# Performance work log

Measured on AMD Instinct MI355X. Metric: run time of the kernel, lower is better.

The kernel has to match this reference:

```python
import jax, jax.numpy as jnp
import numpy as np

N = 50000
E = 800000
IN, HID, OUT = 256, 128, 64
BN_EPS = 1e-5

def sage(x, src, dst, Wl, bl, Wr):
    # PyG SAGEConv (aggr='mean'): lin_l(mean_j x_j) + lin_r(x_root)
    agg = jax.ops.segment_sum(x[src], dst, num_segments=N)
    deg = jax.ops.segment_sum(jnp.ones((src.shape[0], 1), x.dtype), dst, num_segments=N)
    mean_agg = agg / jnp.maximum(deg, 1.0)
    return mean_agg @ Wl + bl + x @ Wr

def bn_eval(x, gamma, beta):
    # eval-mode BatchNorm1d with running_mean=0, running_var=1
    return x * (gamma / jnp.sqrt(1.0 + BN_EPS)) + beta

def setup_inputs() -> dict:
    key = jax.random.key(0)
    ks = jax.random.split(key, 16)
    g = lambda k, shp, s: jax.random.normal(k, shp, jnp.float32) * s
    inp = {
        'x': g(ks[0], (N, IN), 1.0),
        'edge_index': jax.random.randint(ks[1], (2, E), 0, N, jnp.int32),
        'eps': g(ks[2], (10, N, OUT), 1.0),
        'W1l': g(ks[3], (IN, HID), 0.06), 'b1': jnp.zeros((HID,), jnp.float32), 'W1r': g(ks[4], (IN, HID), 0.06),
        'g1': jnp.ones((HID,), jnp.float32), 'be1': jnp.zeros((HID,), jnp.float32),
        'W2l': g(ks[5], (HID, 2 * HID), 0.09), 'b2': jnp.zeros((2 * HID,), jnp.float32), 'W2r': g(ks[6], (HID, 2 * HID), 0.09),
        'g2': jnp.ones((2 * HID,), jnp.float32), 'be2': jnp.zeros((2 * HID,), jnp.float32),
        'W3l': g(ks[7], (2 * HID, 2 * OUT), 0.06), 'b3': jnp.zeros((2 * OUT,), jnp.float32), 'W3r': g(ks[8], (2 * HID, 2 * OUT), 0.06),
        'Wd1': g(ks[9], (OUT, HID), 0.12), 'bd1': jnp.zeros((HID,), jnp.float32),
        'g3': jnp.ones((HID,), jnp.float32), 'be3': jnp.zeros((HID,), jnp.float32),
        'Wd2': g(ks[10], (HID, IN), 0.09), 'bd2': jnp.zeros((IN,), jnp.float32),
    }
    return inp

def reference(x, edge_index, eps, W1l, b1, W1r, g1, be1, W2l, b2, W2r, g2, be2,
              W3l, b3, W3r, Wd1, bd1, g3, be3, Wd2, bd2):
    src, dst = edge_index[0], edge_index[1]
    # encode (dropout is identity in eval mode)
    x1 = bn_eval(jax.nn.relu(sage(x, src, dst, W1l, b1, W1r)), g1, be1)
    x2 = bn_eval(jax.nn.relu(sage(x1, src, dst, W2l, b2, W2r)), g2, be2)
    mz = sage(x2, src, dst, W3l, b3, W3r)
    mean, log_std = mz[:, :OUT], mz[:, OUT:]
    # reparameterize: average of n_samples draws == mean + std * mean(eps)
    std = jnp.exp(log_std)
    z = mean + std * jnp.mean(eps, axis=0)
    # decode
    h = bn_eval(jax.nn.relu(z @ Wd1 + bd1), g3, be3) + x1
    return h @ Wd2 + bd2
```

## Files before the change

kernel.cpp:

```cpp
#include <hip/hip_runtime.h>


typedef unsigned short u16;
typedef short bf16x8 __attribute__((ext_vector_type(8)));
typedef float f32x4  __attribute__((ext_vector_type(4)));

constexpr float BN_EPS = 1e-5f;

__device__ __forceinline__ u16 f2bf(float f) {
    unsigned u = __float_as_uint(f);
    return (u16)((u + 0x7FFFu + ((u >> 16) & 1u)) >> 16);
}
__device__ __forceinline__ float bf2f(u16 h) {
    return __uint_as_float(((unsigned)h) << 16);
}
__device__ __forceinline__ void gl_lds16(const void* g, void* l) {
    __builtin_amdgcn_global_load_lds(
        (const __attribute__((address_space(1))) unsigned*)g,
        (__attribute__((address_space(3))) unsigned*)l, 16, 0, 0);
}

template<int KS>
__device__ __forceinline__ void stage_panel(const u16* g, char* lb, int k0, int t) {
    const int sr   = t >> 2;
    const int sq   = (t & 3) ^ ((t >> 3) & 3);
    const int wave = t >> 6;
    gl_lds16(g + (size_t)sr * KS + k0 + sq * 8,        lb + wave * 1024);
    gl_lds16(g + (size_t)(sr + 64) * KS + k0 + sq * 8, lb + 4096 + wave * 1024);
}


__global__ void histpack(const int* __restrict__ dst, int E, int* __restrict__ deg,
                         const float* __restrict__ x,
                         const float* __restrict__ W1l, const float* __restrict__ W1r,
                         const float* __restrict__ W2l, const float* __restrict__ W2r,
                         const float* __restrict__ W3l, const float* __restrict__ W3r,
                         const float* __restrict__ Wd1, const float* __restrict__ Wd2,
                         u16* __restrict__ Bt1, u16* __restrict__ Bt2,
                         u16* __restrict__ Bt3, u16* __restrict__ Btd1,
                         u16* __restrict__ Btd2, u16* __restrict__ xb,
                         int N, int Mpad) {
    int idx = blockIdx.x * 256 + threadIdx.x;
    if (idx < E) atomicAdd(&deg[dst[idx]], 1);
    if (idx < 65536) {
        int c = idx >> 8, k = idx & 255;
        float v = (c < 128) ? W1l[k * 128 + c] : W1r[k * 128 + (c - 128)];
        Bt1[c * 256 + k] = f2bf(v);
    } else if (idx < 131072) {
        int i2 = idx - 65536;
        int c = i2 >> 8, k = i2 & 255;
        float v = (k < 128) ? W2l[k * 256 + c] : W2r[(k - 128) * 256 + c];
        Bt2[c * 256 + k] = f2bf(v);
    } else if (idx < 196608) {
        int i2 = idx - 131072;
        int c = i2 >> 8, k = i2 & 255;
        float v = (c < 128) ? W3l[k * 128 + c] : W3r[k * 128 + (c - 128)];
        Bt3[c * 256 + k] = f2bf(v);
    } else if (idx < 204800) {
        int i2 = idx - 196608;
        int c = i2 >> 6, k = i2 & 63;
        Btd1[i2] = f2bf(Wd1[k * 128 + c]);
    } else if (idx < 237568) {
        int i2 = idx - 204800;
        int c = i2 >> 7, k = i2 & 127;
        Btd2[i2] = f2bf(Wd2[k * 256 + c]);
    }
    if (idx < Mpad * 64) {
        int row = idx >> 6, q = idx & 63;
        float4 v = make_float4(0.f, 0.f, 0.f, 0.f);
        if (row < N) v = *(const float4*)&x[(size_t)row * 256 + q * 4];
        ushort4 o;
        o.x = f2bf(v.x); o.y = f2bf(v.y); o.z = f2bf(v.z); o.w = f2bf(v.w);
        *(ushort4*)&xb[(size_t)row * 256 + q * 4] = o;
    }
}

__global__ __launch_bounds__(256)
void scan_partial(const int* __restrict__ deg, int N, int* __restrict__ bsum) {
    __shared__ int sd[256];
    int i = blockIdx.x * 256 + threadIdx.x;
    int v = (i < N) ? deg[i] : 0;
    sd[threadIdx.x] = v;
    __syncthreads();
    for (int off = 128; off > 0; off >>= 1) {
        if (threadIdx.x < off) sd[threadIdx.x] += sd[threadIdx.x + off];
        __syncthreads();
    }
    if (threadIdx.x == 0) bsum[blockIdx.x] = sd[0];
}

__global__ __launch_bounds__(256)
void scan_final2(const int* __restrict__ deg, const int* __restrict__ bsum,
                 int N, int E, int* __restrict__ row_ptr, int* __restrict__ cursor,
                 float* __restrict__ inv_deg) {
    __shared__ int sd[256];
    int t = threadIdx.x;
    int partial = 0;
    for (int j = t; j < blockIdx.x; j += 256) partial += bsum[j];
    sd[t] = partial;
    __syncthreads();
    for (int off = 128; off > 0; off >>= 1) {
        if (t < off) sd[t] += sd[t + off];
        __syncthreads();
    }
    int base = sd[0];
    __syncthreads();
    int i = blockIdx.x * 256 + t;
    int d = (i < N) ? deg[i] : 0;
    sd[t] = d;
    __syncthreads();
    for (int off = 1; off < 256; off <<= 1) {
        int u = (t >= off) ? sd[t - off] : 0;
        __syncthreads();
        sd[t] += u;
        __syncthreads();
    }
    if (i < N) {
        int excl = base + sd[t] - d;
        row_ptr[i] = excl;
        cursor[i]  = excl;
        inv_deg[i] = 1.0f / (float)max(d, 1);
        if (i == N - 1) row_ptr[N] = E;
    }
}

__global__ void fill_kernel(const int* __restrict__ src, const int* __restrict__ dst,
                            int E, int* __restrict__ cursor, int* __restrict__ csr) {
    int e = blockIdx.x * 256 + threadIdx.x;
    if (e < E) {
        int p = atomicAdd(&cursor[dst[e]], 1);
        csr[p] = src[e];
    }
}


template<int K, int NC>
__global__ __launch_bounds__(256)
void mgemm(const u16* __restrict__ A, const u16* __restrict__ Bt,
           void* __restrict__ Cout, int M) {
    __shared__ char lds[32768];
    char* As0 = lds;
    char* As1 = lds + 8192;
    char* Bs0 = lds + 16384;
    char* Bs1 = lds + 24576;

    const int t = threadIdx.x;
    const int l = t & 63;
    const int wave = t >> 6;
    const int wr = wave >> 1, wc = wave & 1;
    const int lr = l & 15, kg = l >> 4;
    const int row0 = blockIdx.x * 128;
    const int col0 = blockIdx.y * 128;

    f32x4 acc[4][4];
    #pragma unroll
    for (int m = 0; m < 4; m++)
        #pragma unroll
        for (int n = 0; n < 4; n++)
            #pragma unroll
            for (int r = 0; r < 4; r++) acc[m][n][r] = 0.f;

    const u16* Ab = A  + (size_t)row0 * K;
    const u16* Bb = Bt + (size_t)col0 * K;

    stage_panel<K>(Ab, As0, 0, t);
    stage_panel<K>(Bb, Bs0, 0, t);
    __syncthreads();

    const int swz = (kg ^ ((lr >> 1) & 3)) << 4;
    constexpr int NT = K / 32;
    for (int ks = 0; ks < NT; ks++) {
        char* Ac = (ks & 1) ? As1 : As0;
        char* Bc = (ks & 1) ? Bs1 : Bs0;
        if (ks + 1 < NT) {
            stage_panel<K>(Ab, (ks & 1) ? As0 : As1, (ks + 1) * 32, t);
            stage_panel<K>(Bb, (ks & 1) ? Bs0 : Bs1, (ks + 1) * 32, t);
        }
        bf16x8 af[4], bfr[4];
        #pragma unroll
        for (int m = 0; m < 4; m++)
            af[m] = *(const bf16x8*)(Ac + wr * 4096 + m * 1024 + lr * 64 + swz);
        #pragma unroll
        for (int n = 0; n < 4; n++)
            bfr[n] = *(const bf16x8*)(Bc + wc * 4096 + n * 1024 + lr * 64 + swz);
        #pragma unroll
        for (int m = 0; m < 4; m++)
            #pragma unroll
            for (int n = 0; n < 4; n++)
                acc[m][n] = __builtin_amdgcn_mfma_f32_16x16x32_bf16(
                    af[m], bfr[n], acc[m][n], 0, 0, 0);
        __syncthreads();
    }

    const int colb = col0 + wc * 64;
    const int rowb = row0 + wr * 64;
    __syncthreads();

    char* rp = lds + wave * 4096;
    #pragma unroll
    for (int m = 0; m < 4; m++) {
        #pragma unroll
        for (int n = 0; n < 4; n++)
            #pragma unroll
            for (int r = 0; r < 4; r++) {
                int rl = kg * 4 + r, cl = n * 16 + lr;
                ((u16*)rp)[rl * 64 + cl] = f2bf(acc[m][n][r]);
            }
        u16* rph = (u16*)rp;
        #pragma unroll
        for (int hh = 0; hh < 2; hh++) {
            int rloc = hh * 8 + (l >> 3);
            int grow = rowb + m * 16 + rloc;
            bf16x8 v8 = *(bf16x8*)&rph[rloc * 64 + (l & 7) * 8];
            if (grow < M)
                *(bf16x8*)((u16*)Cout + (size_t)grow * NC + colb + (l & 7) * 8) = v8;
        }
    }
}


__global__ __launch_bounds__(256)
void agg1_kernel(const u16* __restrict__ Y1, const int* __restrict__ row_ptr,
                 const int* __restrict__ csr, const float* __restrict__ inv_deg,
                 const float* __restrict__ b1, const float* __restrict__ g1,
                 const float* __restrict__ be1, u16* __restrict__ catX, int N) {
    int g   = (blockIdx.x * 256 + threadIdx.x) >> 4;
    int sub = threadIdx.x & 15;
    if (g >= N) return;
    int b = row_ptr[g], e = row_ptr[g + 1];
    const int off = sub * 8;
    float a[8] = {};
    int ee = b;
    for (; ee + 3 < e; ee += 4) {
        int j0 = csr[ee], j1 = csr[ee + 1], j2 = csr[ee + 2], j3 = csr[ee + 3];
        bf16x8 v0 = *(const bf16x8*)&Y1[(size_t)j0 * 256 + off];
        bf16x8 v1 = *(const bf16x8*)&Y1[(size_t)j1 * 256 + off];
        bf16x8 v2 = *(const bf16x8*)&Y1[(size_t)j2 * 256 + off];
        bf16x8 v3 = *(const bf16x8*)&Y1[(size_t)j3 * 256 + off];
        #pragma unroll
        for (int r = 0; r < 8; r++)
            a[r] += (bf2f((u16)v0[r]) + bf2f((u16)v1[r]))
                  + (bf2f((u16)v2[r]) + bf2f((u16)v3[r]));
    }
    for (; ee < e; ee++) {
        bf16x8 v0 = *(const bf16x8*)&Y1[(size_t)csr[ee] * 256 + off];
        #pragma unroll
        for (int r = 0; r < 8; r++) a[r] += bf2f((u16)v0[r]);
    }
    float id = inv_deg[g];
    bf16x8 u = *(const bf16x8*)&Y1[(size_t)g * 256 + 128 + off];
    const float rs = rsqrtf(1.0f + BN_EPS);
    bf16x8 o;
    #pragma unroll
    for (int r = 0; r < 8; r++) {
        int c = off + r;
        float v = a[r] * id + b1[c] + bf2f((u16)u[r]);
        v = fmaxf(v, 0.f);
        v = v * (g1[c] * rs) + be1[c];
        o[r] = (short)f2bf(v);
    }
    *(bf16x8*)&catX[(size_t)g * 256 + 128 + off] = o;
}


__global__ __launch_bounds__(256)
void gemm23f(const u16* __restrict__ catX, const u16* __restrict__ Bt2,
             const u16* __restrict__ Bt3,
             const int* __restrict__ row_ptr, const int* __restrict__ csr,
             const float* __restrict__ inv_deg,
             const float* __restrict__ b2, const float* __restrict__ g2,
             const float* __restrict__ be2,
             u16* __restrict__ Y3, int Nn, int M) {
    __shared__ char lds[66560];
    char* At  = lds;
    char* Bd0 = lds + 33792;
    char* Bd1 = lds + 50176;

    const int t = threadIdx.x;
    const int l = t & 63;
    const int wave = t >> 6;
    const int lr = l & 15, kg = l >> 4;
    const int row0 = blockIdx.x * 64;
    const int swz = (kg ^ ((lr >> 1) & 3)) << 4;
    const int sr = t >> 2;
    const int sq = (t & 3) ^ ((t >> 3) & 3);
    const float rs = rsqrtf(1.0f + BN_EPS);

    auto stageB = [&](const u16* Bt, char* buf, int k0) {
        #pragma unroll
        for (int q = 0; q < 4; q++)
            gl_lds16(Bt + (size_t)(q * 64 + sr) * 256 + k0 + sq * 8,
                     buf + q * 4096 + wave * 1024);
    };

    stageB(Bt2, Bd0, 0);

    const int grp = t >> 4, sub = t & 15;
    const int off = sub * 8;
    for (int q = 0; q < 4; q++) {
        int gl = grp * 4 + q;
        int g  = row0 + gl;
        float a[8] = {};
        if (g < Nn) {
            int b = row_ptr[g], e = row_ptr[g + 1];
            int ee = b;
            for (; ee + 3 < e; ee += 4) {
                int j0 = csr[ee], j1 = csr[ee + 1], j2 = csr[ee + 2], j3 = csr[ee + 3];
                bf16x8 v0 = *(const bf16x8*)&catX[(size_t)j0 * 256 + 128 + off];
                bf16x8 v1 = *(const bf16x8*)&catX[(size_t)j1 * 256 + 128 + off];
                bf16x8 v2 = *(const bf16x8*)&catX[(size_t)j2 * 256 + 128 + off];
                bf16x8 v3 = *(const bf16x8*)&catX[(size_t)j3 * 256 + 128 + off];
                #pragma unroll
                for (int r = 0; r < 8; r++)
                    a[r] += (bf2f((u16)v0[r]) + bf2f((u16)v1[r]))
                          + (bf2f((u16)v2[r]) + bf2f((u16)v3[r]));
            }
            for (; ee < e; ee++) {
                bf16x8 v0 = *(const bf16x8*)&catX[(size_t)csr[ee] * 256 + 128 + off];
                #pragma unroll
                for (int r = 0; r < 8; r++) a[r] += bf2f((u16)v0[r]);
            }
            float id = inv_deg[g];
            #pragma unroll
            for (int r = 0; r < 8; r++) a[r] *= id;
        }
        bf16x8 o;
        #pragma unroll
        for (int r = 0; r < 8; r++) o[r] = (short)f2bf(a[r]);
        *(bf16x8*)(At + gl * 528 + sub * 16) = o;
    }
    {
        int row = t >> 2;
        size_t g = (size_t)(row0 + row);
        #pragma unroll
        for (int s = 0; s < 4; s++) {
            int slot = (t & 3) + s * 4;
            bf16x8 v = *(const bf16x8*)&catX[g * 256 + 128 + slot * 8];
            *(bf16x8*)(At + row * 528 + 256 + slot * 16) = v;
        }
    }
    __syncthreads();

    f32x4 acc[4][4];
    #pragma unroll
    for (int m = 0; m < 4; m++)
        #pragma unroll
        for (int n = 0; n < 4; n++)
            #pragma unroll
            for (int r = 0; r < 4; r++) acc[m][n][r] = 0.f;

    for (int ks = 0; ks < 8; ks++) {
        char* Bc = (ks & 1) ? Bd1 : Bd0;
        if (ks < 7) stageB(Bt2, (ks & 1) ? Bd0 : Bd1, (ks + 1) * 32);
        bf16x8 af[4], bfr[4];
        #pragma unroll
        for (int m = 0; m < 4; m++)
            af[m] = *(const bf16x8*)(At + (m * 16 + lr) * 528 + ks * 64 + kg * 16);
        #pragma unroll
        for (int n = 0; n < 4; n++)
            bfr[n] = *(const bf16x8*)(Bc + wave * 4096 + n * 1024 + lr * 64 + swz);
        #pragma unroll
        for (int m = 0; m < 4; m++)
            #pragma unroll
            for (int n = 0; n < 4; n++)
                acc[m][n] = __builtin_amdgcn_mfma_f32_16x16x32_bf16(
                    af[m], bfr[n], acc[m][n], 0, 0, 0);
        __syncthreads();
    }

    stageB(Bt3, Bd0, 0);

    {
        float bia[4], gpr[4], bet[4];
        #pragma unroll
        for (int n = 0; n < 4; n++) {
            int c = wave * 64 + n * 16 + lr;
            bia[n] = b2[c];
            gpr[n] = g2[c] * rs;
            bet[n] = be2[c];
        }
        #pragma unroll
        for (int m = 0; m < 4; m++)
            #pragma unroll
            for (int n = 0; n < 4; n++)
                #pragma unroll
                for (int r = 0; r < 4; r++) {
                    int rl = m * 16 + kg * 4 + r;
                    int cl = wave * 64 + n * 16 + lr;
                    float v = acc[m][n][r] + bia[n];
                    v = fmaxf(v, 0.f) * gpr[n] + bet[n];
                    *(u16*)(At + rl * 528 + cl * 2) = f2bf(v);
                }
    }
    __syncthreads();

    #pragma unroll
    for (int m = 0; m < 4; m++)
        #pragma unroll
        for (int n = 0; n < 4; n++)
            #pragma unroll
            for (int r = 0; r < 4; r++) acc[m][n][r] = 0.f;

    for (int ks = 0; ks < 8; ks++) {
        char* Bc = (ks & 1) ? Bd1 : Bd0;
        if (ks < 7) stageB(Bt3, (ks & 1) ? Bd0 : Bd1, (ks + 1) * 32);
        bf16x8 af[4], bfr[4];
        #pragma unroll
        for (int m = 0; m < 4; m++)
            af[m] = *(const bf16x8*)(At + (m * 16 + lr) * 528 + ks * 64 + kg * 16);
        #pragma unroll
        for (int n = 0; n < 4; n++)
            bfr[n] = *(const bf16x8*)(Bc + wave * 4096 + n * 1024 + lr * 64 + swz);
        #pragma unroll
        for (int m = 0; m < 4; m++)
            #pragma unroll
            for (int n = 0; n < 4; n++)
                acc[m][n] = __builtin_amdgcn_mfma_f32_16x16x32_bf16(
                    af[m], bfr[n], acc[m][n], 0, 0, 0);
        __syncthreads();
    }

    char* rp = lds + wave * 4096;
    #pragma unroll
    for (int m = 0; m < 4; m++) {
        #pragma unroll
        for (int n = 0; n < 4; n++)
            #pragma unroll
            for (int r = 0; r < 4; r++) {
                int rl = kg * 4 + r, cl = n * 16 + lr;
                ((u16*)rp)[rl * 64 + cl] = f2bf(acc[m][n][r]);
            }
        u16* rph = (u16*)rp;
        #pragma unroll
        for (int hh = 0; hh < 2; hh++) {
            int rloc = hh * 8 + (l >> 3);
            int grow = row0 + m * 16 + rloc;
            bf16x8 v8 = *(bf16x8*)&rph[rloc * 64 + (l & 7) * 8];
            if (grow < M)
                *(bf16x8*)&Y3[(size_t)grow * 256 + wave * 64 + (l & 7) * 8] = v8;
        }
    }
}


__global__ __launch_bounds__(256)
void decf(const u16* __restrict__ Y3, const int* __restrict__ row_ptr,
          const int* __restrict__ csr, const float* __restrict__ inv_deg,
          const float* __restrict__ b3, const float* __restrict__ eps,
          const u16* __restrict__ Btd1, const u16* __restrict__ Btd2,
          const float* __restrict__ bd1, const float* __restrict__ g3,
          const float* __restrict__ be3, const u16* __restrict__ x1,
          const float* __restrict__ bd2, float* __restrict__ out,
          int Nn, int M) {
    __shared__ char lds[67584];
    char* zl = lds + 16384;
    char* hb = lds + 34816;
    const int t = threadIdx.x;
    const int l = t & 63;
    const int wave = t >> 6;
    const int wr = wave >> 1, wc = wave & 1;
    const int lr = l & 15, kg = l >> 4;
    const int row0 = blockIdx.x * 128;
    const float rs = rsqrtf(1.0f + BN_EPS);
    const int swz = (kg ^ ((lr >> 1) & 3)) << 4;

    stage_panel<64>(Btd1, lds,        0, t);
    stage_panel<64>(Btd1, lds + 8192, 32, t);

    const int grp = t >> 4, sub = t & 15;
    const int off = sub * 8;
    const int wb = (t & 63) & ~15;
    const int s0 = wb + ((2 * sub) & 15);
    const int s1 = wb + ((2 * sub + 1) & 15);
    for (int q = 0; q < 8; q++) {
        int gl = grp * 8 + q;
        int g  = row0 + gl;
        if (g < Nn) {
            f32x4 emv = {0.f, 0.f, 0.f, 0.f};
            #pragma unroll
            for (int t10 = 0; t10 < 10; t10++) {
                f32x4 v = *(const f32x4*)&eps[((size_t)t10 * Nn + g) * 64 + sub * 4];
                emv += v;
            }
            emv *= 0.1f;

            float a[8] = {};
            int b = row_ptr[g], e = row_ptr[g + 1];
            int ee = b;
            for (; ee + 3 < e; ee += 4) {
                int j0 = csr[ee], j1 = csr[ee + 1], j2 = csr[ee + 2], j3 = csr[ee + 3];
                bf16x8 v0 = *(const bf16x8*)&Y3[(size_t)j0 * 256 + off];
                bf16x8 v1 = *(const bf16x8*)&Y3[(size_t)j1 * 256 + off];
                bf16x8 v2 = *(const bf16x8*)&Y3[(size_t)j2 * 256 + off];
                bf16x8 v3 = *(const bf16x8*)&Y3[(size_t)j3 * 256 + off];
                #pragma unroll
                for (int r = 0; r < 8; r++)
                    a[r] += (bf2f((u16)v0[r]) + bf2f((u16)v1[r]))
                          + (bf2f((u16)v2[r]) + bf2f((u16)v3[r]));
            }
            for (; ee < e; ee++) {
                bf16x8 v0 = *(const bf16x8*)&Y3[(size_t)csr[ee] * 256 + off];
                #pragma unroll
                for (int r = 0; r < 8; r++) a[r] += bf2f((u16)v0[r]);
            }
            float id = inv_deg[g];
            bf16x8 u = *(const bf16x8*)&Y3[(size_t)g * 256 + 128 + off];
            float mzv[8];
            #pragma unroll
            for (int r = 0; r < 8; r++)
                mzv[r] = a[r] * id + b3[off + r] + bf2f((u16)u[r]);

            float em8[8];
            #pragma unroll
            for (int qq = 0; qq < 4; qq++) {
                em8[qq]     = __shfl(emv[qq], s0);
                em8[4 + qq] = __shfl(emv[qq], s1);
            }
            float hi[8];
            #pragma unroll
            for (int r = 0; r < 8; r++) hi[r] = __shfl_xor(mzv[r], 8);

            if (sub < 8) {
                bf16x8 o;
                #pragma unroll
                for (int r = 0; r < 8; r++)
                    o[r] = (short)f2bf(mzv[r] + expf(hi[r]) * em8[r]);
                *(bf16x8*)(zl + gl * 144 + sub * 16) = o;
            }
        } else if (sub < 8) {
            bf16x8 o;
            #pragma unroll
            for (int r = 0; r < 8; r++) o[r] = 0;
            *(bf16x8*)(zl + gl * 144 + sub * 16) = o;
        }
    }
    __syncthreads();

    f32x4 acc[4][4];
    #pragma unroll
    for (int m = 0; m < 4; m++)
        #pragma unroll
        for (int n = 0; n < 4; n++)
            #pragma unroll
            for (int r = 0; r < 4; r++) acc[m][n][r] = 0.f;

    #pragma unroll
    for (int ks = 0; ks < 2; ks++) {
        char* Bc = lds + ks * 8192;
        bf16x8 af[4], bfr[4];
        #pragma unroll
        for (int m = 0; m < 4; m++)
            af[m] = *(const bf16x8*)(zl + (wr * 64 + m * 16 + lr) * 144
                                        + ks * 64 + kg * 16);
        #pragma unroll
        for (int n = 0; n < 4; n++)
            bfr[n] = *(const bf16x8*)(Bc + wc * 4096 + n * 1024 + lr * 64 + swz);
        #pragma unroll
        for (int m = 0; m < 4; m++)
            #pragma unroll
            for (int n = 0; n < 4; n++)
                acc[m][n] = __builtin_amdgcn_mfma_f32_16x16x32_bf16(
                    af[m], bfr[n], acc[m][n], 0, 0, 0);
    }

    {
        float bia[4], gpr[4], bet[4];
        #pragma unroll
        for (int n = 0; n < 4; n++) {
            int c = wc * 64 + n * 16 + lr;
            bia[n] = bd1[c];
            gpr[n] = g3[c] * rs;
            bet[n] = be3[c];
        }
        #pragma unroll
        for (int m = 0; m < 4; m++)
            #pragma unroll
            for (int n = 0; n < 4; n++)
                #pragma unroll
                for (int r = 0; r < 4; r++) {
                    int rl = wr * 64 + m * 16 + kg * 4 + r;
                    int cl = wc * 64 + n * 16 + lr;
                    float v = acc[m][n][r] + bia[n];
                    v = fmaxf(v, 0.f) * gpr[n] + bet[n];
                    v += bf2f(x1[(size_t)(row0 + rl) * 256 + cl]);
                    int slot = (cl >> 3) ^ (rl & 7);
                    ((u16*)(hb + rl * 256 + slot * 16))[cl & 7] = f2bf(v);
                }
    }
    __syncthreads();

    for (int ch = 0; ch < 2; ch++) {
        const u16* Bb2 = Btd2 + ch * 16384;
        stage_panel<128>(Bb2, lds, 0, t);
        #pragma unroll
        for (int m = 0; m < 4; m++)
            #pragma unroll
            for (int n = 0; n < 4; n++)
                #pragma unroll
                for (int r = 0; r < 4; r++) acc[m][n][r] = 0.f;
        __syncthreads();

        for (int ks = 0; ks < 4; ks++) {
            char* Bc = lds + (ks & 1) * 8192;
            if (ks + 1 < 4)
                stage_panel<128>(Bb2, lds + (((ks & 1) ^ 1) * 8192), (ks + 1) * 32, t);
            bf16x8 af[4], bfr[4];
            #pragma unroll
            for (int m = 0; m < 4; m++) {
                int row = wr * 64 + m * 16 + lr;
                int s = (ks * 4 + kg) ^ (row & 7);
                af[m] = *(const bf16x8*)(hb + row * 256 + s * 16);
            }
            #pragma unroll
            for (int n = 0; n < 4; n++)
                bfr[n] = *(const bf16x8*)(Bc + wc * 4096 + n * 1024 + lr * 64 + swz);
            #pragma unroll
            for (int m = 0; m < 4; m++)
                #pragma unroll
                for (int n = 0; n < 4; n++)
                    acc[m][n] = __builtin_amdgcn_mfma_f32_16x16x32_bf16(
                        af[m], bfr[n], acc[m][n], 0, 0, 0);
            __syncthreads();
        }

        const int colb = ch * 128 + wc * 64;
        const int rowb = row0 + wr * 64;
        float b2v[4];
        #pragma unroll
        for (int n = 0; n < 4; n++) b2v[n] = bd2[colb + n * 16 + lr];
        char* rp = lds + wave * 4096;
        #pragma unroll
        for (int m = 0; m < 4; m++) {
            #pragma unroll
            for (int n = 0; n < 4; n++)
                #pragma unroll
                for (int r = 0; r < 4; r++)
                    ((float*)rp)[(kg * 4 + r) * 64 + n * 16 + lr] = acc[m][n][r] + b2v[n];
            float* rpf = (float*)rp;
            #pragma unroll
            for (int rr = 0; rr < 4; rr++) {
                int rloc = rr * 4 + kg;
                int grow = rowb + m * 16 + rloc;
                if (grow < M) {
                    f32x4 v4 = *(f32x4*)&rpf[rloc * 64 + lr * 4];
                    *(f32x4*)&out[(size_t)grow * 256 + colb + lr * 4] = v4;
                }
            }
        }
        __syncthreads();
    }
}


extern "C" void kernel_launch(void* const* d_in, const int* in_sizes, int n_in,
                              void* d_out, int out_size, void* d_ws, size_t ws_size,
                              hipStream_t stream) {
    const float* x    = (const float*)d_in[0];
    const int*   ei   = (const int*)d_in[1];
    const float* eps  = (const float*)d_in[2];
    const float* W1l  = (const float*)d_in[3];
    const float* b1   = (const float*)d_in[4];
    const float* W1r  = (const float*)d_in[5];
    const float* g1   = (const float*)d_in[6];
    const float* be1  = (const float*)d_in[7];
    const float* W2l  = (const float*)d_in[8];
    const float* b2   = (const float*)d_in[9];
    const float* W2r  = (const float*)d_in[10];
    const float* g2   = (const float*)d_in[11];
    const float* be2  = (const float*)d_in[12];
    const float* W3l  = (const float*)d_in[13];
    const float* b3   = (const float*)d_in[14];
    const float* W3r  = (const float*)d_in[15];
    const float* Wd1  = (const float*)d_in[16];
    const float* bd1  = (const float*)d_in[17];
    const float* g3   = (const float*)d_in[18];
    const float* be3  = (const float*)d_in[19];
    const float* Wd2  = (const float*)d_in[20];
    const float* bd2  = (const float*)d_in[21];

    const int Nn   = in_sizes[0] / 256;
    const int E    = in_sizes[1] / 2;
    const int Mpad = ((Nn + 127) / 128) * 128;
    const int* srcp = ei;
    const int* dstp = ei + E;
    const int nb = (Nn + 255) / 256;

    char* w = (char*)d_ws;
    auto alloc = [&](size_t bytes) -> void* {
        void* p = (void*)w;
        w += (bytes + 255) & ~(size_t)255;
        return p;
    };
    int*   deg     = (int*)  alloc((size_t)Nn * 4);
    int*   bsum    = (int*)  alloc((size_t)nb * 4);
    int*   row_ptr = (int*)  alloc((size_t)(Nn + 1) * 4);
    int*   cursor  = (int*)  alloc((size_t)Nn * 4);
    float* inv_deg = (float*)alloc((size_t)Nn * 4);
    int*   csr     = (int*)  alloc((size_t)E * 4);
    u16*   Bt1     = (u16*)  alloc(256 * 256 * 2);
    u16*   Bt2     = (u16*)  alloc(256 * 256 * 2);
    u16*   Bt3     = (u16*)  alloc(256 * 256 * 2);
    u16*   Btd1    = (u16*)  alloc(128 * 64 * 2);
    u16*   Btd2    = (u16*)  alloc(256 * 128 * 2);
    u16*   xb      = (u16*)  alloc((size_t)Mpad * 256 * 2);
    u16*   bufA    = (u16*)  alloc((size_t)Mpad * 256 * 2);
    u16*   bufB    = (u16*)  alloc((size_t)Mpad * 256 * 2);
    u16*   bufC    = (u16*)  alloc((size_t)Mpad * 256 * 2);
    if ((size_t)(w - (char*)d_ws) > ws_size) return;

    hipMemsetAsync(deg, 0, (size_t)Nn * 4, stream);
    histpack<<<(Mpad * 64 + 255) / 256, 256, 0, stream>>>(
        dstp, E, deg, x, W1l, W1r, W2l, W2r, W3l, W3r, Wd1, Wd2,
        Bt1, Bt2, Bt3, Btd1, Btd2, xb, Nn, Mpad);
    scan_partial<<<nb, 256, 0, stream>>>(deg, Nn, bsum);
    scan_final2<<<nb, 256, 0, stream>>>(deg, bsum, Nn, E, row_ptr, cursor, inv_deg);
    fill_kernel<<<(E + 255) / 256, 256, 0, stream>>>(srcp, dstp, E, cursor, csr);

    dim3 g2c(Mpad / 128, 2);
    const int aggBlocks = (Nn + 15) / 16;

    mgemm<256, 256><<<g2c, 256, 0, stream>>>(xb, Bt1, bufA, Mpad);
    agg1_kernel<<<aggBlocks, 256, 0, stream>>>(bufA, row_ptr, csr, inv_deg,
                                               b1, g1, be1, bufB, Nn);
    gemm23f<<<Mpad / 64, 256, 0, stream>>>(bufB, Bt2, Bt3, row_ptr, csr, inv_deg,
                                           b2, g2, be2, bufC, Nn, Mpad);
    decf<<<Mpad / 128, 256, 0, stream>>>(bufC, row_ptr, csr, inv_deg, b3, eps,
                                         Btd1, Btd2, bd1, g3, be3,
                                         bufB + 128, bd2, (float*)d_out, Nn, Nn);
}
```

Before: 328.5 us.

## Split decoder into a wide neighbor-aggregation kernel and a separate GEMM kernel

The third-layer mean aggregation, the eps averaging and the reparameterization move out of the fused decoder kernel into a standalone agg3_kernel. That kernel uses one 16-thread group per node across many small blocks, instead of 128 nodes per block handled serially within a few hundred blocks. It writes z as a bf16 buffer, which the new dec_fused kernel stages into LDS with the same swizzled panel loader it uses for the weights. The aim is more parallelism and better latency hiding for the irregular gather. The cost is an extra kernel launch and a round trip of z through global memory, and padded rows of z are no longer zero-initialized.

Result: faster. 306.5 us (-6.7%).

```diff
diff --git a/kernel.cpp b/kernel.cpp
--- a/kernel.cpp
+++ b/kernel.cpp
@@ -444,17 +444,80 @@
 
 
 __global__ __launch_bounds__(256)
-void decf(const u16* __restrict__ Y3, const int* __restrict__ row_ptr,
-          const int* __restrict__ csr, const float* __restrict__ inv_deg,
-          const float* __restrict__ b3, const float* __restrict__ eps,
-          const u16* __restrict__ Btd1, const u16* __restrict__ Btd2,
-          const float* __restrict__ bd1, const float* __restrict__ g3,
-          const float* __restrict__ be3, const u16* __restrict__ x1,
-          const float* __restrict__ bd2, float* __restrict__ out,
-          int Nn, int M) {
-    __shared__ char lds[67584];
-    char* zl = lds + 16384;
-    char* hb = lds + 34816;
+void agg3_kernel(const u16* __restrict__ Y3, const int* __restrict__ row_ptr,
+                 const int* __restrict__ csr, const float* __restrict__ inv_deg,
+                 const float* __restrict__ b3, const float* __restrict__ eps,
+                 u16* __restrict__ z, int N) {
+    int g   = (blockIdx.x * 256 + threadIdx.x) >> 4;
+    int sub = threadIdx.x & 15;
+    if (g >= N) return;
+    int b = row_ptr[g], e = row_ptr[g + 1];
+    const int off = sub * 8;
+
+    f32x4 emv = {0.f, 0.f, 0.f, 0.f};
+    #pragma unroll
+    for (int t10 = 0; t10 < 10; t10++) {
+        f32x4 v = *(const f32x4*)&eps[((size_t)t10 * N + g) * 64 + sub * 4];
+        emv += v;
+    }
+    emv *= 0.1f;
+
+    float a[8] = {};
+    int ee = b;
+    for (; ee + 3 < e; ee += 4) {
+        int j0 = csr[ee], j1 = csr[ee + 1], j2 = csr[ee + 2], j3 = csr[ee + 3];
+        bf16x8 v0 = *(const bf16x8*)&Y3[(size_t)j0 * 256 + off];
+        bf16x8 v1 = *(const bf16x8*)&Y3[(size_t)j1 * 256 + off];
+        bf16x8 v2 = *(const bf16x8*)&Y3[(size_t)j2 * 256 + off];
+        bf16x8 v3 = *(const bf16x8*)&Y3[(size_t)j3 * 256 + off];
+        #pragma unroll
+        for (int r = 0; r < 8; r++)
+            a[r] += (bf2f((u16)v0[r]) + bf2f((u16)v1[r]))
+                  + (bf2f((u16)v2[r]) + bf2f((u16)v3[r]));
+    }
+    for (; ee < e; ee++) {
+        bf16x8 v0 = *(const bf16x8*)&Y3[(size_t)csr[ee] * 256 + off];
+        #pragma unroll
+        for (int r = 0; r < 8; r++) a[r] += bf2f((u16)v0[r]);
+    }
+    float id = inv_deg[g];
+    bf16x8 u = *(const bf16x8*)&Y3[(size_t)g * 256 + 128 + off];
+    float mzv[8];
+    #pragma unroll
+    for (int r = 0; r < 8; r++)
+        mzv[r] = a[r] * id + b3[off + r] + bf2f((u16)u[r]);
+
+    const int wl = threadIdx.x & 63;
+    const int wb = wl & ~15;
+    const int s0 = wb + ((2 * sub) & 15);
+    const int s1 = wb + ((2 * sub + 1) & 15);
+    float em8[8];
+    #pragma unroll
+    for (int q = 0; q < 4; q++) {
+        em8[q]     = __shfl(emv[q], s0);
+        em8[4 + q] = __shfl(emv[q], s1);
+    }
+    float hi[8];
+    #pragma unroll
+    for (int r = 0; r < 8; r++) hi[r] = __shfl_xor(mzv[r], 8);
+
+    if (sub < 8) {
+        bf16x8 o;
+        #pragma unroll
+        for (int r = 0; r < 8; r++)
+            o[r] = (short)f2bf(mzv[r] + expf(hi[r]) * em8[r]);
+        *(bf16x8*)&z[(size_t)g * 64 + sub * 8] = o;
+    }
+}
+
+
+__global__ __launch_bounds__(256)
+void dec_fused(const u16* __restrict__ zb, const u16* __restrict__ Btd1,
+               const u16* __restrict__ Btd2, const float* __restrict__ bd1,
+               const float* __restrict__ g3, const float* __restrict__ be3,
+               const u16* __restrict__ x1, const float* __restrict__ bd2,
+               float* __restrict__ out, int M) {
+    __shared__ char lds[65536];
     const int t = threadIdx.x;
     const int l = t & 63;
     const int wave = t >> 6;
@@ -463,77 +526,12 @@
     const int row0 = blockIdx.x * 128;
     const float rs = rsqrtf(1.0f + BN_EPS);
     const int swz = (kg ^ ((lr >> 1) & 3)) << 4;
-
-    stage_panel<64>(Btd1, lds,        0, t);
-    stage_panel<64>(Btd1, lds + 8192, 32, t);
-
-    const int grp = t >> 4, sub = t & 15;
-    const int off = sub * 8;
-    const int wb = (t & 63) & ~15;
-    const int s0 = wb + ((2 * sub) & 15);
-    const int s1 = wb + ((2 * sub + 1) & 15);
-    for (int q = 0; q < 8; q++) {
-        int gl = grp * 8 + q;
-        int g  = row0 + gl;
-        if (g < Nn) {
-            f32x4 emv = {0.f, 0.f, 0.f, 0.f};
-            #pragma unroll
-            for (int t10 = 0; t10 < 10; t10++) {
-                f32x4 v = *(const f32x4*)&eps[((size_t)t10 * Nn + g) * 64 + sub * 4];
-                emv += v;
-            }
-            emv *= 0.1f;
-
-            float a[8] = {};
-            int b = row_ptr[g], e = row_ptr[g + 1];
-            int ee = b;
-            for (; ee + 3 < e; ee += 4) {
-                int j0 = csr[ee], j1 = csr[ee + 1], j2 = csr[ee + 2], j3 = csr[ee + 3];
-                bf16x8 v0 = *(const bf16x8*)&Y3[(size_t)j0 * 256 + off];
-                bf16x8 v1 = *(const bf16x8*)&Y3[(size_t)j1 * 256 + off];
-                bf16x8 v2 = *(const bf16x8*)&Y3[(size_t)j2 * 256 + off];
-                bf16x8 v3 = *(const bf16x8*)&Y3[(size_t)j3 * 256 + off];
-                #pragma unroll
-                for (int r = 0; r < 8; r++)
-                    a[r] += (bf2f((u16)v0[r]) + bf2f((u16)v1[r]))
-                          + (bf2f((u16)v2[r]) + bf2f((u16)v3[r]));
-            }
-            for (; ee < e; ee++) {
-                bf16x8 v0 = *(const bf16x8*)&Y3[(size_t)csr[ee] * 256 + off];
-                #pragma unroll
-                for (int r = 0; r < 8; r++) a[r] += bf2f((u16)v0[r]);
-            }
-            float id = inv_deg[g];
-            bf16x8 u = *(const bf16x8*)&Y3[(size_t)g * 256 + 128 + off];
-            float mzv[8];
-            #pragma unroll
-            for (int r = 0; r < 8; r++)
-                mzv[r] = a[r] * id + b3[off + r] + bf2f((u16)u[r]);
-
-            float em8[8];
-            #pragma unroll
-            for (int qq = 0; qq < 4; qq++) {
-                em8[qq]     = __shfl(emv[qq], s0);
-                em8[4 + qq] = __shfl(emv[qq], s1);
-            }
-            float hi[8];
-            #pragma unroll
-            for (int r = 0; r < 8; r++) hi[r] = __shfl_xor(mzv[r], 8);
-
-            if (sub < 8) {
-                bf16x8 o;
-                #pragma unroll
-                for (int r = 0; r < 8; r++)
-                    o[r] = (short)f2bf(mzv[r] + expf(hi[r]) * em8[r]);
-                *(bf16x8*)(zl + gl * 144 + sub * 16) = o;
-            }
-        } else if (sub < 8) {
-            bf16x8 o;
-            #pragma unroll
-            for (int r = 0; r < 8; r++) o[r] = 0;
-            *(bf16x8*)(zl + gl * 144 + sub * 16) = o;
-        }
-    }
+    char* hb = lds + 32768;
+
+    stage_panel<64>(zb + (size_t)row0 * 64, lds,         0, t);
+    stage_panel<64>(zb + (size_t)row0 * 64, lds + 8192, 32, t);
+    stage_panel<64>(Btd1, lds + 16384,  0, t);
+    stage_panel<64>(Btd1, lds + 24576, 32, t);
     __syncthreads();
 
     f32x4 acc[4][4];
@@ -546,12 +544,12 @@
 
     #pragma unroll
     for (int ks = 0; ks < 2; ks++) {
-        char* Bc = lds + ks * 8192;
+        char* Ac = lds + ks * 8192;
+        char* Bc = lds + 16384 + ks * 8192;
         bf16x8 af[4], bfr[4];
         #pragma unroll
         for (int m = 0; m < 4; m++)
-            af[m] = *(const bf16x8*)(zl + (wr * 64 + m * 16 + lr) * 144
-                                        + ks * 64 + kg * 16);
+            af[m] = *(const bf16x8*)(Ac + wr * 4096 + m * 1024 + lr * 64 + swz);
         #pragma unroll
         for (int n = 0; n < 4; n++)
             bfr[n] = *(const bf16x8*)(Bc + wc * 4096 + n * 1024 + lr * 64 + swz);
@@ -703,6 +701,7 @@
     u16*   Btd1    = (u16*)  alloc(128 * 64 * 2);
     u16*   Btd2    = (u16*)  alloc(256 * 128 * 2);
     u16*   xb      = (u16*)  alloc((size_t)Mpad * 256 * 2);
+    u16*   zb      = (u16*)  alloc((size_t)Mpad * 64 * 2);
     u16*   bufA    = (u16*)  alloc((size_t)Mpad * 256 * 2);
     u16*   bufB    = (u16*)  alloc((size_t)Mpad * 256 * 2);
     u16*   bufC    = (u16*)  alloc((size_t)Mpad * 256 * 2);
@@ -724,7 +723,8 @@
                                                b1, g1, be1, bufB, Nn);
     gemm23f<<<Mpad / 64, 256, 0, stream>>>(bufB, Bt2, Bt3, row_ptr, csr, inv_deg,
                                            b2, g2, be2, bufC, Nn, Mpad);
-    decf<<<Mpad / 128, 256, 0, stream>>>(bufC, row_ptr, csr, inv_deg, b3, eps,
-                                         Btd1, Btd2, bd1, g3, be3,
-                                         bufB + 128, bd2, (float*)d_out, Nn, Nn);
-}
+    agg3_kernel<<<aggBlocks, 256, 0, stream>>>(bufC, row_ptr, csr, inv_deg,
+                                               b3, eps, zb, Nn);
+    dec_fused<<<Mpad / 128, 256, 0, stream>>>(
+        zb, Btd1, Btd2, bd1, g3, be3, bufB + 128, bd2, (float*)d_out, Nn);
+}
```
